# Kernel tuning notes

Hardware: AMD Instinct MI355X
Metric: run time of the kernel (lower is better)

## Reference

```python
import jax, jax.numpy as jnp
import numpy as np

TEMPERATURE = 0.07
EPS = 1e-8          # torch cosine_similarity norm clamp
DIAG_FILL = 9e-15   # value masked_fill'ed onto the diagonal BEFORE temperature scaling


def setup_inputs() -> dict:
    key = jax.random.key(0)
    N, D = 16384, 128
    feats = jax.random.normal(key, (N, D), dtype=jnp.float32)
    # unique labels: required for the original torch code's broadcast
    # (-cos_sim[pos_mask] must have exactly N elements)
    labels = jnp.arange(N, dtype=jnp.int32).reshape(N, 1)
    return {"feats": feats, "labels": labels}


def reference(feats, labels):
    # cosine similarity matrix: normalize rows once, then a single GEMM
    norm = jnp.maximum(jnp.linalg.norm(feats, axis=-1, keepdims=True), EPS)
    f = feats / norm
    cos_sim = f @ f.T                                   # [N, N]

    N = cos_sim.shape[0]
    eye = jnp.eye(N, dtype=bool)
    cos_sim = jnp.where(eye, DIAG_FILL, cos_sim)        # masked_fill_(self_mask, 9e-15)
    cos_sim = cos_sim / TEMPERATURE

    pos_mask = labels == labels.T                       # [N, N] bool, one True per row
    # cos_sim[pos_mask] with exactly one positive per row == masked row-sum
    pos = jnp.sum(jnp.where(pos_mask, cos_sim, 0.0), axis=-1)  # [N]

    nll = -pos + jax.nn.logsumexp(cos_sim, axis=-1)     # [N]
    return jnp.mean(nll)
```

## Files before the change

kernel.cpp:

```cpp
#include <hip/hip_runtime.h>
#include <hip/hip_bf16.h>
#include <stdint.h>

typedef __attribute__((ext_vector_type(8))) short short8;
typedef __attribute__((ext_vector_type(4))) float f32x4;

#define N_ROWS 16384
#define DIM 128
#define NPAIR 64
#define SUBS 8
#define TRI_BLOCKS (NPAIR * SUBS)
#define TOTAL_CHUNKS 8256

constexpr float ALPHA = 4.5398160f;
constexpr float POSC  = 1.2857143e-13f;
constexpr float LN2   = 0.69314718056f;

__global__ void normalize_kernel(const float* __restrict__ feats,
                                 unsigned short* __restrict__ G,
                                 float* __restrict__ rowsum,
                                 unsigned int* __restrict__ cnts) {
  const int tid  = threadIdx.x;
  const int lane = tid & 63;
  const int row  = blockIdx.x * 4 + (tid >> 6);

  const float2 v = *(const float2*)(feats + (size_t)row * DIM + lane * 2);
  float ss = v.x * v.x + v.y * v.y;
#pragma unroll
  for (int m = 1; m < 64; m <<= 1) ss += __shfl_xor(ss, m);
  const float sc = ALPHA / fmaxf(sqrtf(ss), 1e-8f);

  __hip_bfloat16 h0 = __float2bfloat16(v.x * sc);
  __hip_bfloat16 h1 = __float2bfloat16(v.y * sc);
  unsigned int packed = (unsigned int)(*(unsigned short*)&h0) |
                        ((unsigned int)(*(unsigned short*)&h1) << 16);
  *(unsigned int*)(G + (size_t)row * DIM + lane * 2) = packed;

  if (blockIdx.x < 64) rowsum[blockIdx.x * 256 + tid] = 0.f;
  if (blockIdx.x == 0 && tid < 4) cnts[tid] = 0u;
}

__global__ __launch_bounds__(256, 2) void simclr_tri_kernel(
    const unsigned short* __restrict__ G, float* __restrict__ rowsum,
    float* __restrict__ colbuf) {
  const int tid  = threadIdx.x;
  const int lane = tid & 63;
  const int w    = tid >> 6;
  const int c    = lane & 15;
  const int q    = lane >> 4;

  const int p     = blockIdx.x / SUBS;
  const int sub   = blockIdx.x % SUBS;
  const int start = (sub * 129) / SUBS;
  const int end   = ((sub + 1) * 129) / SUBS;

  __shared__ __align__(16) unsigned short Bbuf[128 * 128];
  __shared__ float ldsCol[2][128];

  ((float*)ldsCol)[tid] = 0.f;

  unsigned goff[8];
#pragma unroll
  for (int t = 0; t < 8; ++t) {
    const int cidx = t * 256 + tid;
    const int col  = cidx >> 4;
    const int kc   = (cidx & 15) ^ (col & 15);
    goff[t] = (unsigned)(col * DIM + kc * 8);
  }
  unsigned colb[8];
#pragma unroll
  for (int tc = 0; tc < 8; ++tc) colb[tc] = (unsigned)((tc * 16 + c) * 256);

  const short* Gs = (const short*)G;
  const char*  bb = (const char*)Bbuf;
  const f32x4 zero4 = {0.f, 0.f, 0.f, 0.f};

  short8 afrag[2][4];
  short8 breg[8];
  float rs[2][4];
  int cur_rt = -1, prev_g = -1;

  {
    const int i0  = start;
    const int ct0 = (i0 < 128 - p) ? p + i0 : i0 - 1;
    const unsigned short* gsrc = G + ((size_t)ct0 << 14);
#pragma unroll
    for (int t = 0; t < 8; ++t)
      breg[t] = *(const short8*)(gsrc + goff[t]);
  }

#pragma unroll 1
  for (int i = start; i < end; ++i) {
    const int rt = (i < 128 - p) ? p : 127 - p;
    const int ct = (i < 128 - p) ? p + i : i - 1;
    const int g  = p * 129 + i;
    const bool offd = (rt != ct);
    const int it = i - start;

    __syncthreads();

    if (prev_g >= 0 && tid < 128) {
      const int pf = (it + 1) & 1;
      colbuf[(size_t)prev_g * 128 + tid] = ldsCol[pf][tid];
      ldsCol[pf][tid] = 0.f;
    }

    const bool newA = (rt != cur_rt);
    if (newA && cur_rt >= 0) {
#pragma unroll
      for (int tr = 0; tr < 2; ++tr)
#pragma unroll
        for (int r = 0; r < 4; ++r) {
          float v = rs[tr][r];
          v += __shfl_xor(v, 1); v += __shfl_xor(v, 2);
          v += __shfl_xor(v, 4); v += __shfl_xor(v, 8);
          if (c == 0)
            atomicAdd(&rowsum[cur_rt * 128 + w * 32 + tr * 16 + q * 4 + r], v);
        }
    }

#pragma unroll
    for (int t = 0; t < 8; ++t)
      *(short8*)(&Bbuf[(size_t)(t * 256 + tid) * 8]) = breg[t];

    if (newA) {
      const short* ap = Gs + ((size_t)(rt * 128 + w * 32 + c) << 7) + q * 8;
#pragma unroll
      for (int tr = 0; tr < 2; ++tr)
#pragma unroll
        for (int ks = 0; ks < 4; ++ks)
          afrag[tr][ks] = *(const short8*)(ap + tr * 16 * 128 + ks * 32);
#pragma unroll
      for (int tr = 0; tr < 2; ++tr)
#pragma unroll
        for (int r = 0; r < 4; ++r) rs[tr][r] = 0.f;
      cur_rt = rt;
    }
    __syncthreads();

    if (i + 1 < end) {
      const int i1  = i + 1;
      const int nct = (i1 < 128 - p) ? p + i1 : i1 - 1;
      const unsigned short* gsrc = G + ((size_t)nct << 14);
#pragma unroll
      for (int t = 0; t < 8; ++t)
        breg[t] = *(const short8*)(gsrc + goff[t]);
    }

    f32x4 acc[2][8];
#pragma unroll
    for (int ks = 0; ks < 4; ++ks) {
      const unsigned kx = (unsigned)(((ks * 4 + q) ^ c) * 16);
#pragma unroll
      for (int half = 0; half < 2; ++half) {
        short8 bfr[4];
#pragma unroll
        for (int jj = 0; jj < 4; ++jj)
          bfr[jj] = *(const short8*)(bb + colb[half * 4 + jj] + kx);
#pragma unroll
        for (int tr = 0; tr < 2; ++tr)
#pragma unroll
          for (int jj = 0; jj < 4; ++jj) {
            const int tc = half * 4 + jj;
            acc[tr][tc] = __builtin_amdgcn_mfma_f32_16x16x32_bf16(
                afrag[tr][ks], bfr[jj],
                (ks == 0) ? zero4 : acc[tr][tc], 0, 0, 0);
          }
      }
    }

    if (!offd) {
#pragma unroll
      for (int tr = 0; tr < 2; ++tr) {
        const int dtc = w * 2 + tr;
#pragma unroll
        for (int tc = 0; tc < 8; ++tc)
#pragma unroll
          for (int r = 0; r < 4; ++r)
            acc[tr][tc][r] =
                (tc == dtc && c == q * 4 + r) ? 0.f : acc[tr][tc][r];
      }
    }

    float cs[8];
#pragma unroll
    for (int tc = 0; tc < 8; ++tc) cs[tc] = 0.f;
#pragma unroll
    for (int tr = 0; tr < 2; ++tr)
#pragma unroll
      for (int tc = 0; tc < 8; ++tc) {
        const float e0 = __builtin_amdgcn_exp2f(acc[tr][tc][0]);
        const float e1 = __builtin_amdgcn_exp2f(acc[tr][tc][1]);
        const float e2 = __builtin_amdgcn_exp2f(acc[tr][tc][2]);
        const float e3 = __builtin_amdgcn_exp2f(acc[tr][tc][3]);
        rs[tr][0] += e0; rs[tr][1] += e1; rs[tr][2] += e2; rs[tr][3] += e3;
        cs[tc] += (e0 + e1) + (e2 + e3);
      }
    if (offd) {
#pragma unroll
      for (int tc = 0; tc < 8; ++tc) {
        float v = cs[tc];
        v += __shfl_xor(v, 16); v += __shfl_xor(v, 32);
        if (q == 0) atomicAdd(&ldsCol[it & 1][tc * 16 + c], v);
      }
    }
    prev_g = offd ? g : -1;
  }

  const int itn = end - start;
  __syncthreads();
  if (prev_g >= 0 && tid < 128)
    colbuf[(size_t)prev_g * 128 + tid] = ldsCol[(itn + 1) & 1][tid];
  if (cur_rt >= 0) {
#pragma unroll
    for (int tr = 0; tr < 2; ++tr)
#pragma unroll
      for (int r = 0; r < 4; ++r) {
        float v = rs[tr][r];
        v += __shfl_xor(v, 1); v += __shfl_xor(v, 2);
        v += __shfl_xor(v, 4); v += __shfl_xor(v, 8);
        if (c == 0)
          atomicAdd(&rowsum[cur_rt * 128 + w * 32 + tr * 16 + q * 4 + r], v);
      }
  }
}

__global__ void colreduce_finalize_kernel(const float* __restrict__ colbuf,
                                          const float* __restrict__ rowsum,
                                          unsigned int* __restrict__ cnts,
                                          float* __restrict__ out) {
  const int tid  = threadIdx.x;
  const int lane = tid & 63;
  const int wv   = tid >> 6;
  const int col  = tid & 127;
  const int part = tid >> 7;
  const int T    = blockIdx.x;

  const int lo = part ? (T >> 1) : 0;
  const int hi = part ? T : (T >> 1);

  float s = 0.f;
  for (int rt = lo; rt < hi; ++rt) {
    const int g = (rt < 64) ? (rt * 129 + (T - rt))
                            : ((127 - rt) * 129 + (T + 1));
    s += colbuf[(size_t)g * 128 + col];
  }

  __shared__ float acc[128];
  __shared__ float wpart[4];
  __shared__ int finFlag;
  if (part == 1) acc[col] = s;
  __syncthreads();

  float l = 0.f;
  if (part == 0) {
    const float tot = s + acc[col] + rowsum[T * 128 + col];
    l = __builtin_amdgcn_logf(tot);
  }
#pragma unroll
  for (int m = 1; m < 64; m <<= 1) l += __shfl_xor(l, m);
  if (lane == 0) wpart[wv] = l;
  __syncthreads();
  if (tid == 0) {
    const float bsum = wpart[0] + wpart[1] + wpart[2] + wpart[3];
    atomicAdd((float*)&cnts[2], bsum);
    __threadfence();
    finFlag = (atomicAdd(&cnts[1], 1u) == 127u) ? 1 : 0;
  }
  __syncthreads();
  if (finFlag && tid == 0) {
    const float lsum = __hip_atomic_load((float*)&cnts[2], __ATOMIC_RELAXED,
                                         __HIP_MEMORY_SCOPE_AGENT);
    out[0] = lsum * LN2 / (float)N_ROWS - POSC;
  }
}

extern "C" void kernel_launch(void* const* d_in, const int* in_sizes, int n_in,
                              void* d_out, int out_size, void* d_ws, size_t ws_size,
                              hipStream_t stream) {
  (void)in_sizes; (void)n_in; (void)out_size; (void)ws_size;
  const float* feats = (const float*)d_in[0];
  char* ws = (char*)d_ws;
  unsigned short* G = (unsigned short*)ws;
  float* rowsum = (float*)(ws + (size_t)N_ROWS * DIM * 2);
  unsigned int* cnts =
      (unsigned int*)(ws + (size_t)N_ROWS * DIM * 2 + (size_t)N_ROWS * 4);
  float* colbuf =
      (float*)(ws + (size_t)N_ROWS * DIM * 2 + (size_t)N_ROWS * 4 + 256);

  normalize_kernel<<<dim3(N_ROWS / 4), dim3(256), 0, stream>>>(feats, G, rowsum, cnts);
  simclr_tri_kernel<<<dim3(TRI_BLOCKS), dim3(256), 0, stream>>>(G, rowsum, colbuf);
  colreduce_finalize_kernel<<<dim3(128), dim3(256), 0, stream>>>(
      colbuf, rowsum, cnts, (float*)d_out);
}
```

Baseline: 145.6 us.

## Drop LDS B staging, use 2x2 wave tiling with register-prefetched B fragments

The triangular GEMM kernel no longer stages the B tile through shared memory. Each wave now owns a 64x64 sub-tile in a 2x2 wave grid and loads its B fragments straight from global memory, prefetching the next k-slice and the next tile in registers. This removes the LDS writes, one barrier per tile and the LDS reads, but relies on L2/L1 to serve the duplicated B loads and raises per-wave register use. The column-reduce kernel is also split across 4x more blocks that atomically add into rowsum, and the last block computes every log in a serial pass over all 16384 rows.

Result: slower. 167.2 us (+14.8%).

```diff
diff --git a/kernel.cpp b/kernel.cpp
--- a/kernel.cpp
+++ b/kernel.cpp
@@ -7,10 +7,8 @@
 
 #define N_ROWS 16384
 #define DIM 128
-#define NPAIR 64
 #define SUBS 8
-#define TRI_BLOCKS (NPAIR * SUBS)
-#define TOTAL_CHUNKS 8256
+#define TRI_BLOCKS 512
 
 constexpr float ALPHA = 4.5398160f;
 constexpr float POSC  = 1.2857143e-13f;
@@ -46,6 +44,8 @@
   const int tid  = threadIdx.x;
   const int lane = tid & 63;
   const int w    = tid >> 6;
+  const int wr   = w >> 1;
+  const int wc   = w & 1;
   const int c    = lane & 15;
   const int q    = lane >> 4;
 
@@ -54,39 +54,25 @@
   const int start = (sub * 129) / SUBS;
   const int end   = ((sub + 1) * 129) / SUBS;
 
-  __shared__ __align__(16) unsigned short Bbuf[128 * 128];
   __shared__ float ldsCol[2][128];
-
   ((float*)ldsCol)[tid] = 0.f;
 
-  unsigned goff[8];
-#pragma unroll
-  for (int t = 0; t < 8; ++t) {
-    const int cidx = t * 256 + tid;
-    const int col  = cidx >> 4;
-    const int kc   = (cidx & 15) ^ (col & 15);
-    goff[t] = (unsigned)(col * DIM + kc * 8);
-  }
-  unsigned colb[8];
-#pragma unroll
-  for (int tc = 0; tc < 8; ++tc) colb[tc] = (unsigned)((tc * 16 + c) * 256);
-
-  const short* Gs = (const short*)G;
-  const char*  bb = (const char*)Bbuf;
-  const f32x4 zero4 = {0.f, 0.f, 0.f, 0.f};
-
-  short8 afrag[2][4];
-  short8 breg[8];
-  float rs[2][4];
+  const short* Gs   = (const short*)G;
+  const int    koff = q * 8;
+  const f32x4  zero4 = {0.f, 0.f, 0.f, 0.f};
+
+  short8 afrag[4][4];
+  short8 bcur[4];
+  float  rs[4][4];
   int cur_rt = -1, prev_g = -1;
 
   {
     const int i0  = start;
     const int ct0 = (i0 < 128 - p) ? p + i0 : i0 - 1;
-    const unsigned short* gsrc = G + ((size_t)ct0 << 14);
-#pragma unroll
-    for (int t = 0; t < 8; ++t)
-      breg[t] = *(const short8*)(gsrc + goff[t]);
+    const short* bp = Gs + ((size_t)(ct0 * 128 + wc * 64 + c) << 7) + koff;
+#pragma unroll
+    for (int tc = 0; tc < 4; ++tc)
+      bcur[tc] = *(const short8*)(bp + ((tc * 16) << 7));
   }
 
 #pragma unroll 1
@@ -106,89 +92,75 @@
     }
 
     const bool newA = (rt != cur_rt);
-    if (newA && cur_rt >= 0) {
-#pragma unroll
-      for (int tr = 0; tr < 2; ++tr)
-#pragma unroll
-        for (int r = 0; r < 4; ++r) {
-          float v = rs[tr][r];
-          v += __shfl_xor(v, 1); v += __shfl_xor(v, 2);
-          v += __shfl_xor(v, 4); v += __shfl_xor(v, 8);
-          if (c == 0)
-            atomicAdd(&rowsum[cur_rt * 128 + w * 32 + tr * 16 + q * 4 + r], v);
-        }
-    }
-
-#pragma unroll
-    for (int t = 0; t < 8; ++t)
-      *(short8*)(&Bbuf[(size_t)(t * 256 + tid) * 8]) = breg[t];
-
     if (newA) {
-      const short* ap = Gs + ((size_t)(rt * 128 + w * 32 + c) << 7) + q * 8;
-#pragma unroll
-      for (int tr = 0; tr < 2; ++tr)
+      if (cur_rt >= 0) {
+#pragma unroll
+        for (int tr = 0; tr < 4; ++tr)
+#pragma unroll
+          for (int r = 0; r < 4; ++r) {
+            float v = rs[tr][r];
+            v += __shfl_xor(v, 1); v += __shfl_xor(v, 2);
+            v += __shfl_xor(v, 4); v += __shfl_xor(v, 8);
+            if (c == 0)
+              atomicAdd(&rowsum[cur_rt * 128 + wr * 64 + tr * 16 + q * 4 + r], v);
+          }
+      }
+      const short* ap = Gs + ((size_t)(rt * 128 + wr * 64 + c) << 7) + koff;
+#pragma unroll
+      for (int tr = 0; tr < 4; ++tr)
 #pragma unroll
         for (int ks = 0; ks < 4; ++ks)
-          afrag[tr][ks] = *(const short8*)(ap + tr * 16 * 128 + ks * 32);
-#pragma unroll
-      for (int tr = 0; tr < 2; ++tr)
+          afrag[tr][ks] = *(const short8*)(ap + ((tr * 16) << 7) + ks * 32);
+#pragma unroll
+      for (int tr = 0; tr < 4; ++tr)
 #pragma unroll
         for (int r = 0; r < 4; ++r) rs[tr][r] = 0.f;
       cur_rt = rt;
     }
-    __syncthreads();
-
-    if (i + 1 < end) {
-      const int i1  = i + 1;
-      const int nct = (i1 < 128 - p) ? p + i1 : i1 - 1;
-      const unsigned short* gsrc = G + ((size_t)nct << 14);
-#pragma unroll
-      for (int t = 0; t < 8; ++t)
-        breg[t] = *(const short8*)(gsrc + goff[t]);
-    }
-
-    f32x4 acc[2][8];
+
+    const short* bp = Gs + ((size_t)(ct * 128 + wc * 64 + c) << 7) + koff;
+    f32x4 acc[4][4];
 #pragma unroll
     for (int ks = 0; ks < 4; ++ks) {
-      const unsigned kx = (unsigned)(((ks * 4 + q) ^ c) * 16);
-#pragma unroll
-      for (int half = 0; half < 2; ++half) {
-        short8 bfr[4];
-#pragma unroll
-        for (int jj = 0; jj < 4; ++jj)
-          bfr[jj] = *(const short8*)(bb + colb[half * 4 + jj] + kx);
-#pragma unroll
-        for (int tr = 0; tr < 2; ++tr)
-#pragma unroll
-          for (int jj = 0; jj < 4; ++jj) {
-            const int tc = half * 4 + jj;
-            acc[tr][tc] = __builtin_amdgcn_mfma_f32_16x16x32_bf16(
-                afrag[tr][ks], bfr[jj],
-                (ks == 0) ? zero4 : acc[tr][tc], 0, 0, 0);
-          }
-      }
-    }
-
-    if (!offd) {
-#pragma unroll
-      for (int tr = 0; tr < 2; ++tr) {
-        const int dtc = w * 2 + tr;
-#pragma unroll
-        for (int tc = 0; tc < 8; ++tc)
-#pragma unroll
-          for (int r = 0; r < 4; ++r)
-            acc[tr][tc][r] =
-                (tc == dtc && c == q * 4 + r) ? 0.f : acc[tr][tc][r];
-      }
-    }
-
-    float cs[8];
-#pragma unroll
-    for (int tc = 0; tc < 8; ++tc) cs[tc] = 0.f;
-#pragma unroll
-    for (int tr = 0; tr < 2; ++tr)
-#pragma unroll
-      for (int tc = 0; tc < 8; ++tc) {
+      short8 bnext[4];
+      if (ks < 3) {
+#pragma unroll
+        for (int tc = 0; tc < 4; ++tc)
+          bnext[tc] = *(const short8*)(bp + ((tc * 16) << 7) + (ks + 1) * 32);
+      } else if (i + 1 < end) {
+        const int i1  = i + 1;
+        const int ct1 = (i1 < 128 - p) ? p + i1 : i1 - 1;
+        const short* bp1 = Gs + ((size_t)(ct1 * 128 + wc * 64 + c) << 7) + koff;
+#pragma unroll
+        for (int tc = 0; tc < 4; ++tc)
+          bnext[tc] = *(const short8*)(bp1 + ((tc * 16) << 7));
+      } else {
+#pragma unroll
+        for (int tc = 0; tc < 4; ++tc) bnext[tc] = bcur[tc];
+      }
+#pragma unroll
+      for (int tr = 0; tr < 4; ++tr)
+#pragma unroll
+        for (int tc = 0; tc < 4; ++tc)
+          acc[tr][tc] = __builtin_amdgcn_mfma_f32_16x16x32_bf16(
+              afrag[tr][ks], bcur[tc], (ks == 0) ? zero4 : acc[tr][tc], 0, 0, 0);
+#pragma unroll
+      for (int tc = 0; tc < 4; ++tc) bcur[tc] = bnext[tc];
+    }
+
+    if (!offd && wr == wc) {
+#pragma unroll
+      for (int tr = 0; tr < 4; ++tr)
+#pragma unroll
+        for (int r = 0; r < 4; ++r)
+          acc[tr][tr][r] = (c == q * 4 + r) ? 0.f : acc[tr][tr][r];
+    }
+
+    float cs[4] = {0.f, 0.f, 0.f, 0.f};
+#pragma unroll
+    for (int tr = 0; tr < 4; ++tr)
+#pragma unroll
+      for (int tc = 0; tc < 4; ++tc) {
         const float e0 = __builtin_amdgcn_exp2f(acc[tr][tc][0]);
         const float e1 = __builtin_amdgcn_exp2f(acc[tr][tc][1]);
         const float e2 = __builtin_amdgcn_exp2f(acc[tr][tc][2]);
@@ -198,10 +170,10 @@
       }
     if (offd) {
 #pragma unroll
-      for (int tc = 0; tc < 8; ++tc) {
+      for (int tc = 0; tc < 4; ++tc) {
         float v = cs[tc];
         v += __shfl_xor(v, 16); v += __shfl_xor(v, 32);
-        if (q == 0) atomicAdd(&ldsCol[it & 1][tc * 16 + c], v);
+        if (q == 0) atomicAdd(&ldsCol[it & 1][wc * 64 + tc * 16 + c], v);
       }
     }
     prev_g = offd ? g : -1;
@@ -213,20 +185,20 @@
     colbuf[(size_t)prev_g * 128 + tid] = ldsCol[(itn + 1) & 1][tid];
   if (cur_rt >= 0) {
 #pragma unroll
-    for (int tr = 0; tr < 2; ++tr)
+    for (int tr = 0; tr < 4; ++tr)
 #pragma unroll
       for (int r = 0; r < 4; ++r) {
         float v = rs[tr][r];
         v += __shfl_xor(v, 1); v += __shfl_xor(v, 2);
         v += __shfl_xor(v, 4); v += __shfl_xor(v, 8);
         if (c == 0)
-          atomicAdd(&rowsum[cur_rt * 128 + w * 32 + tr * 16 + q * 4 + r], v);
+          atomicAdd(&rowsum[cur_rt * 128 + wr * 64 + tr * 16 + q * 4 + r], v);
       }
   }
 }
 
 __global__ void colreduce_finalize_kernel(const float* __restrict__ colbuf,
-                                          const float* __restrict__ rowsum,
+                                          float* __restrict__ rowsum,
                                           unsigned int* __restrict__ cnts,
                                           float* __restrict__ out) {
   const int tid  = threadIdx.x;
@@ -234,10 +206,11 @@
   const int wv   = tid >> 6;
   const int col  = tid & 127;
   const int part = tid >> 7;
-  const int T    = blockIdx.x;
-
-  const int lo = part ? (T >> 1) : 0;
-  const int hi = part ? T : (T >> 1);
+  const int T    = blockIdx.x >> 2;
+  const int seg  = (blockIdx.x & 3) * 2 + part;
+
+  const int lo = (T * seg) >> 3;
+  const int hi = (T * (seg + 1)) >> 3;
 
   float s = 0.f;
   for (int rt = lo; rt < hi; ++rt) {
@@ -245,33 +218,31 @@
                             : ((127 - rt) * 129 + (T + 1));
     s += colbuf[(size_t)g * 128 + col];
   }
-
-  __shared__ float acc[128];
+  if (hi > lo) atomicAdd(&rowsum[T * 128 + col], s);
+
+  __shared__ int finFlag;
   __shared__ float wpart[4];
-  __shared__ int finFlag;
-  if (part == 1) acc[col] = s;
-  __syncthreads();
-
-  float l = 0.f;
-  if (part == 0) {
-    const float tot = s + acc[col] + rowsum[T * 128 + col];
-    l = __builtin_amdgcn_logf(tot);
-  }
-#pragma unroll
-  for (int m = 1; m < 64; m <<= 1) l += __shfl_xor(l, m);
-  if (lane == 0) wpart[wv] = l;
   __syncthreads();
   if (tid == 0) {
-    const float bsum = wpart[0] + wpart[1] + wpart[2] + wpart[3];
-    atomicAdd((float*)&cnts[2], bsum);
     __threadfence();
-    finFlag = (atomicAdd(&cnts[1], 1u) == 127u) ? 1 : 0;
+    finFlag = (atomicAdd(&cnts[1], 1u) == (unsigned)(4 * 128) - 1u) ? 1 : 0;
   }
   __syncthreads();
-  if (finFlag && tid == 0) {
-    const float lsum = __hip_atomic_load((float*)&cnts[2], __ATOMIC_RELAXED,
-                                         __HIP_MEMORY_SCOPE_AGENT);
-    out[0] = lsum * LN2 / (float)N_ROWS - POSC;
+  if (finFlag) {
+    float lsum = 0.f;
+    for (int i = tid; i < N_ROWS; i += 256) {
+      const float v = __hip_atomic_load(&rowsum[i], __ATOMIC_RELAXED,
+                                        __HIP_MEMORY_SCOPE_AGENT);
+      lsum += __builtin_amdgcn_logf(v);
+    }
+#pragma unroll
+    for (int m = 1; m < 64; m <<= 1) lsum += __shfl_xor(lsum, m);
+    if (lane == 0) wpart[wv] = lsum;
+    __syncthreads();
+    if (tid == 0) {
+      const float ssum = wpart[0] + wpart[1] + wpart[2] + wpart[3];
+      out[0] = ssum * LN2 / (float)N_ROWS - POSC;
+    }
   }
 }
 
@@ -290,6 +261,6 @@
 
   normalize_kernel<<<dim3(N_ROWS / 4), dim3(256), 0, stream>>>(feats, G, rowsum, cnts);
   simclr_tri_kernel<<<dim3(TRI_BLOCKS), dim3(256), 0, stream>>>(G, rowsum, colbuf);
-  colreduce_finalize_kernel<<<dim3(128), dim3(256), 0, stream>>>(
+  colreduce_finalize_kernel<<<dim3(512), dim3(256), 0, stream>>>(
       colbuf, rowsum, cnts, (float*)d_out);
 }
```
